# Kernel optimization log

Measured on AMD Instinct MI355X. Metric: run time of the kernel, lower is better.

The kernel has to match this reference:

```python
import jax, jax.numpy as jnp
import numpy as np

B, L, DIN, H, N, TEMB, NB = 16, 1024, 64, 256, 64, 128, 6


def setup_inputs() -> dict:
    key = jax.random.key(0)
    ks = jax.random.split(key, 16)
    def nrm(k, shape, scale):
        return jax.random.normal(k, shape, dtype=jnp.float32) * scale
    inp = {}
    inp["input"] = nrm(ks[0], (B, L, DIN), 1.0)
    inp["t"] = jax.random.uniform(ks[1], (B,), dtype=jnp.float32) * 1000.0
    inp["W_in"] = nrm(ks[2], (DIN, H), DIN ** -0.5)
    inp["b_in"] = jnp.zeros((H,), jnp.float32)
    inp["Wt1"] = nrm(ks[3], (TEMB, H), TEMB ** -0.5)
    inp["bt1"] = jnp.zeros((H,), jnp.float32)
    inp["Wt2"] = nrm(ks[4], (H, H), H ** -0.5)
    inp["bt2"] = jnp.zeros((H,), jnp.float32)
    inp["ln_g"] = jnp.ones((NB, H), jnp.float32)
    inp["ln_b"] = jnp.zeros((NB, H), jnp.float32)
    lo, hi = float(np.log(0.001)), float(np.log(0.1))
    inp["log_dt"] = jax.random.uniform(ks[5], (NB, H), dtype=jnp.float32) * (hi - lo) + lo
    inp["A_log_re"] = jnp.full((NB, H, N), float(np.log(0.5)), jnp.float32)
    inp["A_im"] = jnp.broadcast_to(np.pi * jnp.arange(N, dtype=jnp.float32), (NB, H, N)) + 0.0
    inp["C_re"] = nrm(ks[6], (NB, 2, H, N), 0.5 ** 0.5)
    inp["C_im"] = nrm(ks[7], (NB, 2, H, N), 0.5 ** 0.5)
    inp["Dp"] = nrm(ks[8], (NB, H), 1.0)
    inp["s4W"] = nrm(ks[9], (NB, H, H), H ** -0.5)
    inp["s4b"] = jnp.zeros((NB, H), jnp.float32)
    inp["tW"] = nrm(ks[10], (NB, H, H), H ** -0.5)
    inp["tb"] = jnp.zeros((NB, H), jnp.float32)
    inp["c1W"] = nrm(ks[11], (NB, H, H), H ** -0.5)
    inp["c1b"] = jnp.zeros((NB, H), jnp.float32)
    inp["c2W"] = nrm(ks[12], (NB, H, H), H ** -0.5)
    inp["c2b"] = jnp.zeros((NB, H), jnp.float32)
    inp["Wo1"] = nrm(ks[13], (H, H), H ** -0.5)
    inp["bo1"] = jnp.zeros((H,), jnp.float32)
    inp["Wo2"] = nrm(ks[14], (H, DIN), H ** -0.5)
    inp["bo2"] = jnp.zeros((DIN,), jnp.float32)
    return inp


def _sin_emb(t, dim):
    half = dim // 2
    freqs = jnp.exp(-np.log(10000.0) / (half - 1) * jnp.arange(half, dtype=jnp.float32))
    a = t[:, None] * freqs[None, :]
    return jnp.concatenate([jnp.sin(a), jnp.cos(a)], axis=-1)


def _forward(input, t, W_in, b_in, Wt1, bt1, Wt2, bt2, ln_g, ln_b, log_dt, A_log_re,
             A_im, C_re, C_im, Dp, s4W, s4b, tW, tb, c1W, c1b, c2W, c2b, Wo1, bo1, Wo2, bo2):
    x = jax.nn.relu(input @ W_in + b_in)                     # [B,L,H]
    tv = jax.nn.silu(_sin_emb(t, TEMB) @ Wt1 + bt1)
    tv = jax.nn.silu(tv @ Wt2 + bt2)                         # [B,H]
    x = jnp.swapaxes(x, -1, -2)                              # [B,H,L]
    length = x.shape[-1]
    nfft = 2 * length
    lgrid = jnp.arange(length)
    skips = jnp.zeros_like(x)
    for i in range(NB):
        # time conditioning (broadcast over L)
        tt = tv @ tW[i] + tb[i]                              # [B,H]
        z = x + tt[:, :, None]
        # LayerNorm over channel dim H
        zt = jnp.swapaxes(z, -1, -2)                         # [B,L,H]
        mu = zt.mean(-1, keepdims=True)
        var = zt.var(-1, keepdims=True)
        zn = (zt - mu) / jnp.sqrt(var + 1e-5) * ln_g[i] + ln_b[i]
        zn = jnp.swapaxes(zn, -1, -2)                        # [B,H,L]
        # S4 (diagonal ZOH) bidirectional convolution kernel
        dt = jnp.exp(log_dt[i])                              # [H]
        A = -jnp.exp(A_log_re[i]) + 1j * A_im[i]             # [H,N]
        dtA = A * dt[:, None]
        C = C_re[i] + 1j * C_im[i]                           # [2,H,N]
        dC = C * (jnp.exp(dtA) - 1.0) / A
        V = jnp.exp(dtA[:, :, None] * lgrid)                 # [H,N,L] Vandermonde
        K = 2.0 * jnp.einsum('shn,hnl->shl', dC, V).real     # [2,H,L]
        k = jnp.pad(K[0], ((0, 0), (0, length))) + jnp.pad(K[1][:, ::-1], ((0, 0), (length, 0)))
        y = jnp.fft.irfft(jnp.fft.rfft(zn, nfft) * jnp.fft.rfft(k, nfft)[None], nfft)[..., :length]
        y = y + zn * Dp[i][None, :, None]
        y = jax.nn.gelu(y, approximate=False)
        y = jnp.einsum('oh,bhl->bol', s4W[i], y) + s4b[i][None, :, None]
        out = y + z                                          # S4Layer residual
        g = jnp.tanh(out) * jax.nn.sigmoid(out)
        x = jnp.einsum('oh,bhl->bol', c1W[i], g) + c1b[i][None, :, None] + x
        skips = skips + jnp.einsum('oh,bhl->bol', c2W[i], g) + c2b[i][None, :, None]
    skip = jnp.swapaxes(skips, -1, -2)                       # [B,L,H]
    h = jax.nn.relu(skip @ Wo1 + bo1)
    out = h @ Wo2 + bo2
    return out + input                                       # init_skip


def reference(input, t, W_in, b_in, Wt1, bt1, Wt2, bt2, ln_g, ln_b, log_dt, A_log_re,
              A_im, C_re, C_im, Dp, s4W, s4b, tW, tb, c1W, c1b, c2W, c2b, Wo1, bo1, Wo2, bo2):
    return _forward(input, t, W_in, b_in, Wt1, bt1, Wt2, bt2, ln_g, ln_b, log_dt, A_log_re,
                    A_im, C_re, C_im, Dp, s4W, s4b, tW, tb, c1W, c1b, c2W, c2b, Wo1, bo1, Wo2, bo2)
```

## Files before the change

kernel.cpp:

```cpp
#include <hip/hip_runtime.h>
#include <math.h>


typedef __attribute__((ext_vector_type(8))) short bf16x8;
typedef __attribute__((ext_vector_type(4))) float f32x4;

__device__ __forceinline__ short f2bf(float f) {
  unsigned u = __builtin_bit_cast(unsigned, f);
  unsigned r = (u + 0x7FFFu + ((u >> 16) & 1u)) >> 16;
  return (short)r;
}
__device__ __forceinline__ float bf2f(unsigned short v) {
  unsigned u = ((unsigned)v) << 16;
  return __builtin_bit_cast(float, u);
}

__global__ __launch_bounds__(256) void k_temb(
    const float* __restrict__ t, const float* __restrict__ Wt1, const float* __restrict__ bt1,
    const float* __restrict__ Wt2, const float* __restrict__ bt2, float* __restrict__ tv) {
  int b = blockIdx.x, tid = threadIdx.x;
  __shared__ float emb[128];
  __shared__ float tv1[256];
  if (tid < 128) {
    int j = tid & 63;
    float f = expf(-logf(10000.f) / 63.f * (float)j);
    float a = t[b] * f;
    emb[tid] = (tid < 64) ? sinf(a) : cosf(a);
  }
  __syncthreads();
  float acc = bt1[tid];
  for (int k = 0; k < 128; k++) acc = fmaf(emb[k], Wt1[k * 256 + tid], acc);
  tv1[tid] = acc / (1.f + expf(-acc));
  __syncthreads();
  float acc2 = bt2[tid];
  for (int k = 0; k < 256; k++) acc2 = fmaf(tv1[k], Wt2[k * 256 + tid], acc2);
  tv[b * 256 + tid] = acc2 / (1.f + expf(-acc2));
}

__global__ __launch_bounds__(256) void k_tt(
    const float* __restrict__ tv, const float* __restrict__ tW, const float* __restrict__ tb,
    float* __restrict__ tt_all) {
  int i = blockIdx.x, b = blockIdx.y, h = threadIdx.x;
  __shared__ float s[256];
  s[h] = tv[b * 256 + h];
  __syncthreads();
  const float* W = tW + i * 256 * 256;
  float acc = tb[i * 256 + h];
  for (int k = 0; k < 256; k++) acc = fmaf(s[k], W[k * 256 + h], acc);
  tt_all[(i * 16 + b) * 256 + h] = acc;
}

__global__ __launch_bounds__(256) void k_in(
    const float* __restrict__ inp, const float* __restrict__ W, const float* __restrict__ bias,
    float* __restrict__ x) {
  int lt = blockIdx.x, b = blockIdx.y, h = threadIdx.x;
  __shared__ float si[64][68];
  int l0 = lt * 64;
  for (int rep = 0; rep < 16; rep++) {
    int idx = rep * 256 + h;
    int l = idx >> 6, d = idx & 63;
    si[l][d] = inp[(size_t)(b * 1024 + l0 + l) * 64 + d];
  }
  float wc[64];
  #pragma unroll
  for (int d = 0; d < 64; d++) wc[d] = W[d * 256 + h];
  float bh = bias[h];
  __syncthreads();
  float* xp = x + (size_t)(b * 256 + h) * 1024 + l0;
  for (int l4 = 0; l4 < 16; l4++) {
    float4 o;
    float* op = &o.x;
    #pragma unroll
    for (int j = 0; j < 4; j++) {
      int l = l4 * 4 + j;
      float a = bh;
      #pragma unroll
      for (int d4 = 0; d4 < 16; d4++) {
        float4 v = *reinterpret_cast<const float4*>(&si[l][d4 * 4]);
        a = fmaf(v.x, wc[d4 * 4 + 0], a);
        a = fmaf(v.y, wc[d4 * 4 + 1], a);
        a = fmaf(v.z, wc[d4 * 4 + 2], a);
        a = fmaf(v.w, wc[d4 * 4 + 3], a);
      }
      op[j] = fmaxf(a, 0.f);
    }
    *reinterpret_cast<float4*>(xp + l4 * 4) = o;
  }
}

__global__ __launch_bounds__(256) void k_tab(
    const float* __restrict__ log_dt, const float* __restrict__ A_log_re, const float* __restrict__ A_im,
    const float* __restrict__ C_re, const float* __restrict__ C_im,
    float* __restrict__ wtab, float* __restrict__ wTtab, float* __restrict__ dCtab) {
  int idx = blockIdx.x * 256 + threadIdx.x;
  int i = idx / (256 * 64);
  int rem = idx % (256 * 64);
  int h = rem >> 6, n = rem & 63;
  float dt = expf(log_dt[i * 256 + h]);
  float Ar = -expf(A_log_re[idx]);
  float Ai = A_im[idx];
  float ar = dt * Ar, ai = dt * Ai;
  float ea = expf(ar);
  float wr = ea * cosf(ai), wi = ea * sinf(ai);
  float pr = wr, pi = wi;
  #pragma unroll
  for (int s = 0; s < 6; s++) { float nr = pr * pr - pi * pi; float ni = 2.f * pr * pi; pr = nr; pi = ni; }
  float den = Ar * Ar + Ai * Ai;
  float qr = ((wr - 1.f) * Ar + wi * Ai) / den;
  float qi = (wi * Ar - (wr - 1.f) * Ai) / den;
  wtab[idx * 2] = wr; wtab[idx * 2 + 1] = wi;
  wTtab[idx * 2] = pr; wTtab[idx * 2 + 1] = pi;
  #pragma unroll
  for (int s = 0; s < 2; s++) {
    float cr = C_re[((size_t)(i * 2 + s) * 256 + h) * 64 + n];
    float ci = C_im[((size_t)(i * 2 + s) * 256 + h) * 64 + n];
    dCtab[(((size_t)(i * 2 + s) * 256 + h) * 64 + n) * 2]     = cr * qr - ci * qi;
    dCtab[(((size_t)(i * 2 + s) * 256 + h) * 64 + n) * 2 + 1] = cr * qi + ci * qr;
  }
}

__global__ __launch_bounds__(256) void k_prep(
    const float* __restrict__ s4W, const float* __restrict__ c1W, const float* __restrict__ c2W,
    const float* __restrict__ Wo1,
    unsigned short* __restrict__ s4Wbf, unsigned short* __restrict__ c12Wbf, unsigned short* __restrict__ Wo1T) {
  int idx = blockIdx.x * 256 + threadIdx.x;
  if (idx < 393216) {
    s4Wbf[idx] = (unsigned short)f2bf(s4W[idx]);
  } else if (idx < 393216 + 786432) {
    int j = idx - 393216;
    int i = j / 131072, r = j % 131072;
    int o2 = r >> 8, k = r & 255;
    float v = (o2 < 256) ? c1W[(size_t)i * 65536 + o2 * 256 + k]
                         : c2W[(size_t)i * 65536 + (o2 - 256) * 256 + k];
    c12Wbf[j] = (unsigned short)f2bf(v);
  } else {
    int j = idx - 1179648;
    int o = j >> 8, k = j & 255;
    Wo1T[j] = (unsigned short)f2bf(Wo1[k * 256 + o]);
  }
}

__global__ __launch_bounds__(256) void k_conv(const float* __restrict__ src, unsigned short* __restrict__ dst) {
  int idx = (blockIdx.x * 256 + threadIdx.x) * 8;
  float4 v0 = *reinterpret_cast<const float4*>(src + idx);
  float4 v1 = *reinterpret_cast<const float4*>(src + idx + 4);
  ushort4 a = make_ushort4((unsigned short)f2bf(v0.x), (unsigned short)f2bf(v0.y),
                           (unsigned short)f2bf(v0.z), (unsigned short)f2bf(v0.w));
  ushort4 b = make_ushort4((unsigned short)f2bf(v1.x), (unsigned short)f2bf(v1.y),
                           (unsigned short)f2bf(v1.z), (unsigned short)f2bf(v1.w));
  *reinterpret_cast<ushort4*>(dst + idx) = a;
  *reinterpret_cast<ushort4*>(dst + idx + 4) = b;
}

__global__ __launch_bounds__(256) void k_pcar(const float* __restrict__ wtab, float* __restrict__ Pt) {
  int idx = blockIdx.x * 256 + threadIdx.x;
  int i = idx >> 14, h = (idx >> 6) & 255, n = idx & 63;
  float wr = wtab[idx * 2], wi = wtab[idx * 2 + 1];
  float pr = 1.f, pi = 0.f;
  float* base = Pt + (size_t)i * 2097152 + (size_t)h * 8192 + 2 * n;
  for (int t = 0; t < 64; t++) {
    *reinterpret_cast<float2*>(base + t * 128) = make_float2(pr, -pi);
    float nr2 = pr * wr - pi * wi, ni2 = pr * wi + pi * wr;
    pr = nr2; pi = ni2;
  }
}

__global__ __launch_bounds__(256) void k_ktap(
    const float* __restrict__ dCtab, const float* __restrict__ Pt, float* __restrict__ Ktap) {
  int idx = blockIdx.x * 256 + threadIdx.x;
  int j = idx & 63;
  int h = (idx >> 6) & 255;
  int i = idx >> 15;
  const float* dc = dCtab + (size_t)(idx >> 6) * 128;
  const float* P = Pt + (size_t)i * 2097152 + (size_t)h * 8192 + j * 128;
  float acc = 0.f;
  for (int q = 0; q < 32; q++) {
    float4 d = *reinterpret_cast<const float4*>(dc + q * 4);
    float4 p = *reinterpret_cast<const float4*>(P + q * 4);
    acc = fmaf(d.x, p.x, fmaf(d.y, p.y, fmaf(d.z, p.z, fmaf(d.w, p.w, acc))));
  }
  Ktap[idx] = 2.f * acc;
}

__global__ __launch_bounds__(256) void k_ln(
    const float* __restrict__ x, const float* __restrict__ tt_all,
    const float* __restrict__ g, const float* __restrict__ bta, unsigned short* __restrict__ znbf, int i) {
  int ct = blockIdx.x, b = blockIdx.y, tid = threadIdx.x;
  __shared__ float tile[64][257];
  __shared__ float stt[256];
  __shared__ float red[8][64];
  __shared__ float mu_s[64], rs_s[64];
  stt[tid] = tt_all[(i * 16 + b) * 256 + tid];
  __syncthreads();
  int l0 = ct * 64;
  const float* xb = x + (size_t)(b * 256) * 1024 + l0;
  for (int rep = 0; rep < 16; rep++) {
    int idx = rep * 256 + tid;
    int h = idx >> 4;
    int l4 = (idx & 15) * 4;
    float4 v = *reinterpret_cast<const float4*>(xb + (size_t)h * 1024 + l4);
    float a = stt[h];
    tile[l4][h] = v.x + a; tile[l4 + 1][h] = v.y + a; tile[l4 + 2][h] = v.z + a; tile[l4 + 3][h] = v.w + a;
  }
  __syncthreads();
  int l = tid & 63, part = tid >> 6;
  float s1 = 0.f, s2 = 0.f;
  for (int k = 0; k < 64; k++) {
    float v = tile[l][part * 64 + k];
    s1 += v; s2 = fmaf(v, v, s2);
  }
  red[part][l] = s1; red[4 + part][l] = s2;
  __syncthreads();
  if (tid < 64) {
    float a = red[0][tid] + red[1][tid] + red[2][tid] + red[3][tid];
    float q = red[4][tid] + red[5][tid] + red[6][tid] + red[7][tid];
    float mu = a * (1.f / 256.f);
    float var = q * (1.f / 256.f) - mu * mu;
    mu_s[tid] = mu;
    rs_s[tid] = rsqrtf(var + 1e-5f);
  }
  __syncthreads();
  unsigned short* zb = znbf + (size_t)(b * 256) * 1024 + l0;
  for (int rep = 0; rep < 16; rep++) {
    int idx = rep * 256 + tid;
    int h = idx >> 4;
    int l4 = (idx & 15) * 4;
    float gg = g[i * 256 + h], bb2 = bta[i * 256 + h];
    float o0 = (tile[l4][h]     - mu_s[l4])     * rs_s[l4]     * gg + bb2;
    float o1 = (tile[l4 + 1][h] - mu_s[l4 + 1]) * rs_s[l4 + 1] * gg + bb2;
    float o2 = (tile[l4 + 2][h] - mu_s[l4 + 2]) * rs_s[l4 + 2] * gg + bb2;
    float o3 = (tile[l4 + 3][h] - mu_s[l4 + 3]) * rs_s[l4 + 3] * gg + bb2;
    ushort4 o4 = make_ushort4((unsigned short)f2bf(o0), (unsigned short)f2bf(o1),
                              (unsigned short)f2bf(o2), (unsigned short)f2bf(o3));
    *reinterpret_cast<ushort4*>(zb + (size_t)h * 1024 + l4) = o4;
  }
}

__global__ __launch_bounds__(512, 2) void k_bsc(
    const unsigned short* __restrict__ znbf, const float* __restrict__ Pt,
    const float* __restrict__ wtab, const float* __restrict__ wTtab, const float* __restrict__ dCtab,
    unsigned short* __restrict__ Bl, int i) {
  int h = blockIdx.x;
  int tid = threadIdx.x;
  __shared__ float Ps[64][130];
  __shared__ unsigned short Bp[256][72];
  {
    const float* src = Pt + (size_t)h * 8192;
    #pragma unroll
    for (int rep = 0; rep < 4; rep++) {
      int idx = rep * 512 + tid;
      int t = idx >> 5, k4 = (idx & 31) * 4;
      float4 v = *reinterpret_cast<const float4*>(src + t * 128 + k4);
      *reinterpret_cast<float4*>(&Ps[t][k4]) = v;
    }
  }
  __syncthreads();
  {
    int t = tid & 63;
    int colblk = tid >> 6;
    #pragma unroll
    for (int cc = 0; cc < 32; cc++) {
      int col = colblk * 32 + cc;
      int n = col & 63, comp = (col >> 6) & 1, dir = col >> 7;
      int k = 2 * n + comp;
      float v = dir ? Ps[t][k] : Ps[63 - t][k];
      if (comp) v = -v;
      Bp[col][t] = (unsigned short)f2bf(v);
    }
  }
  __syncthreads();

  int wid = tid >> 6, lane = tid & 63;
  int b = blockIdx.y * 8 + wid;
  int c = lane & 15, kq = lane >> 4;
  const unsigned short* pzn = znbf + ((size_t)(b * 256 + h)) * 1024 + c * 64 + kq * 8;

  bf16x8 af[2];
  af[0] = *reinterpret_cast<const bf16x8*>(pzn);
  af[1] = *reinterpret_cast<const bf16x8*>(pzn + 32);

  f32x4 acc[16];
  #pragma unroll
  for (int nt = 0; nt < 16; nt++) acc[nt] = (f32x4){0.f, 0.f, 0.f, 0.f};
  #pragma unroll
  for (int ks = 0; ks < 2; ks++) {
    #pragma unroll
    for (int nt = 0; nt < 16; nt++) {
      bf16x8 bfv = *reinterpret_cast<const bf16x8*>(&Bp[nt * 16 + c][ks * 32 + kq * 8]);
      acc[nt] = __builtin_amdgcn_mfma_f32_16x16x32_bf16(af[ks], bfv, acc[nt], 0, 0, 0);
    }
  }

  const int gib = (i * 256 + h) * 64;
  unsigned short* blf = Bl + ((size_t)(b * 256 + h)) * 2048;
  unsigned short* blb = blf + (size_t)4096 * 2048;

  #pragma unroll
  for (int j = 0; j < 4; j++) {
    int n = j * 16 + c;
    int gi = gib + n;
    float wTr = wTtab[gi * 2], wTi = wTtab[gi * 2 + 1];
    float w2r = wTr * wTr - wTi * wTi, w2i = 2.f * wTr * wTi;
    float w4r = w2r * w2r - w2i * w2i, w4i = 2.f * w2r * w2i;
    float w8r = w4r * w4r - w4i * w4i, w8i = 2.f * w4r * w4i;
    float wr = wtab[gi * 2], wi = wtab[gi * 2 + 1];
    float d0r = dCtab[((size_t)(i * 2 + 0) * 256 + h) * 128 + 2 * n];
    float d0i = dCtab[((size_t)(i * 2 + 0) * 256 + h) * 128 + 2 * n + 1];
    float d1r = dCtab[((size_t)(i * 2 + 1) * 256 + h) * 128 + 2 * n];
    float d1i = dCtab[((size_t)(i * 2 + 1) * 256 + h) * 128 + 2 * n + 1];
    float mfr = 2.f * (d0r * wr - d0i * wi), mfi = 2.f * (d0r * wi + d0i * wr);
    float mbr = 2.f * d1r, mbi = 2.f * d1i;

    {
      float er = 0.f, ei = 0.f, entr[4], enti[4];
      #pragma unroll
      for (int r = 0; r < 4; r++) {
        entr[r] = er; enti[r] = ei;
        float br = acc[j][r], bi = acc[j + 4][r];
        float t0 = er * wTr - ei * wTi + br;
        ei = er * wTi + ei * wTr + bi; er = t0;
      }
      float Gr = er, Gi = ei;
      float sr = __shfl_up(Gr, 16), si = __shfl_up(Gi, 16);
      if (kq >= 1) { Gr += sr * w4r - si * w4i; Gi += sr * w4i + si * w4r; }
      sr = __shfl_up(Gr, 32); si = __shfl_up(Gi, 32);
      if (kq >= 2) { Gr += sr * w8r - si * w8i; Gi += sr * w8i + si * w8r; }
      float Sgr = __shfl_up(Gr, 16), Sgi = __shfl_up(Gi, 16);
      if (kq == 0) { Sgr = 0.f; Sgi = 0.f; }
      float pr = 1.f, pi = 0.f;
      #pragma unroll
      for (int r = 0; r < 4; r++) {
        float scr = pr * Sgr - pi * Sgi + entr[r];
        float sci = pr * Sgi + pi * Sgr + enti[r];
        float opr = mfr * scr - mfi * sci;
        float opi = mfr * sci + mfi * scr;
        *reinterpret_cast<ushort2*>(blf + (size_t)(kq * 4 + r) * 128 + 2 * n) =
            make_ushort2((unsigned short)f2bf(opr), (unsigned short)f2bf(opi));
        float t0 = pr * wTr - pi * wTi; pi = pr * wTi + pi * wTr; pr = t0;
      }
    }
    {
      float er = 0.f, ei = 0.f, entr[4], enti[4];
      #pragma unroll
      for (int rr = 0; rr < 4; rr++) {
        int r = 3 - rr;
        entr[r] = er; enti[r] = ei;
        float br = acc[8 + j][r], bi = acc[12 + j][r];
        float t0 = er * wTr - ei * wTi + br;
        ei = er * wTi + ei * wTr + bi; er = t0;
      }
      float Gr = er, Gi = ei;
      float sr = __shfl_down(Gr, 16), si = __shfl_down(Gi, 16);
      if (kq <= 2) { Gr += sr * w4r - si * w4i; Gi += sr * w4i + si * w4r; }
      sr = __shfl_down(Gr, 32); si = __shfl_down(Gi, 32);
      if (kq <= 1) { Gr += sr * w8r - si * w8i; Gi += sr * w8i + si * w8r; }
      float Sgr = __shfl_down(Gr, 16), Sgi = __shfl_down(Gi, 16);
      if (kq == 3) { Sgr = 0.f; Sgi = 0.f; }
      float pr = 1.f, pi = 0.f;
      #pragma unroll
      for (int rr = 0; rr < 4; rr++) {
        int r = 3 - rr;
        float scr = pr * Sgr - pi * Sgi + entr[r];
        float sci = pr * Sgi + pi * Sgr + enti[r];
        float opr = mbr * scr - mbi * sci;
        float opi = mbr * sci + mbi * scr;
        *reinterpret_cast<ushort2*>(blb + (size_t)(kq * 4 + r) * 128 + 2 * n) =
            make_ushort2((unsigned short)f2bf(opr), (unsigned short)f2bf(opi));
        float t0 = pr * wTr - pi * wTi; pi = pr * wTi + pi * wTr; pr = t0;
      }
    }
  }
}

__global__ __launch_bounds__(512) void k_apply(
    const unsigned short* __restrict__ znbf, const unsigned short* __restrict__ Bl,
    const float* __restrict__ Pt, const float* __restrict__ Ktap, const float* __restrict__ Dp,
    unsigned short* __restrict__ ygbf, int i) {
  int h = blockIdx.x;
  int tid = threadIdx.x;
  __shared__ short Blds[64][344];
  __shared__ float k0s[64], k1s[64];
  if (tid < 64) k0s[tid] = Ktap[(0 * 256 + h) * 64 + tid];
  else if (tid < 128) k1s[tid - 64] = Ktap[(1 * 256 + h) * 64 + (tid - 64)];
  __syncthreads();
  {
    int trow = tid >> 6, klane = tid & 63;
    const float* Pth = Pt + (size_t)h * 8192;
    #pragma unroll
    for (int ti = 0; ti < 8; ti++) {
      int t = ti * 8 + trow;
      #pragma unroll
      for (int kc = 0; kc < 5; kc++) {
        int k = kc * 64 + klane;
        float v;
        if (kc < 2)      v = Pth[t * 128 + k];
        else if (kc < 4) v = Pth[(63 - t) * 128 + (k - 128)];
        else {
          int tp = klane;
          v = (t >= tp) ? k0s[t - tp] : k1s[tp - t - 1];
        }
        Blds[t][k] = f2bf(v);
      }
    }
  }
  __syncthreads();

  int wid = tid >> 6, lane = tid & 63;
  int b = blockIdx.y * 8 + wid;
  int c = lane & 15, kq = lane >> 4;
  const unsigned short* pa0 = Bl + ((size_t)(b * 256 + h)) * 2048 + c * 128 + kq * 8;
  const unsigned short* pa1 = pa0 + (size_t)4096 * 2048;
  const unsigned short* pzn = znbf + ((size_t)(b * 256 + h)) * 1024 + c * 64 + kq * 8;

  f32x4 acc[4];
  #pragma unroll
  for (int nt = 0; nt < 4; nt++) acc[nt] = (f32x4){0.f, 0.f, 0.f, 0.f};

  #pragma unroll
  for (int ks = 0; ks < 10; ks++) {
    bf16x8 af;
    if (ks < 4)       af = *reinterpret_cast<const bf16x8*>(pa0 + ks * 32);
    else if (ks < 8)  af = *reinterpret_cast<const bf16x8*>(pa1 + (ks - 4) * 32);
    else              af = *reinterpret_cast<const bf16x8*>(pzn + (ks - 8) * 32);
    #pragma unroll
    for (int nt = 0; nt < 4; nt++) {
      bf16x8 bfv = *reinterpret_cast<const bf16x8*>(&Blds[nt * 16 + c][ks * 32 + kq * 8]);
      acc[nt] = __builtin_amdgcn_mfma_f32_16x16x32_bf16(af, bfv, acc[nt], 0, 0, 0);
    }
  }

  float dp = Dp[i * 256 + h];
  size_t obase = (size_t)(b * 256 + h) * 1024;
  #pragma unroll
  for (int nt = 0; nt < 4; nt++) {
    #pragma unroll
    for (int r = 0; r < 4; r++) {
      int m = kq * 4 + r;
      int t = nt * 16 + c;
      size_t idx = obase + (size_t)m * 64 + t;
      float z = bf2f(znbf[idx]);
      float v = fmaf(z, dp, acc[nt][r]);
      float gel = 0.5f * v * (1.f + erff(v * 0.70710678118f));
      ygbf[idx] = (unsigned short)f2bf(gel);
    }
  }
}

template <int EPI>
__global__ __launch_bounds__(256) void k_gemm(
    const unsigned short* __restrict__ Wbf, const float* __restrict__ bias1, const float* __restrict__ bias2,
    const unsigned short* __restrict__ act, float* __restrict__ out1, float* __restrict__ out2,
    unsigned short* __restrict__ outb, const float* __restrict__ aux1, const float* __restrict__ aux2) {
  int lt = blockIdx.x, ot = blockIdx.y, b = blockIdx.z;
  int tid = threadIdx.x;
  int l0 = lt * 128, o0 = ot * 64;
  __shared__ unsigned short Alds[128 * 40];

  int wid = tid >> 6, lane = tid & 63;
  int wo = wid >> 1, wl = wid & 1;
  int c = lane & 15, kq = lane >> 4;

  int kq4 = tid >> 5;
  int lq = tid & 31;
  const unsigned short* actb = act + (size_t)(b * 256) * 1024 + l0 + lq * 4;

  f32x4 acc[2][4];
  #pragma unroll
  for (int mo = 0; mo < 2; mo++)
    #pragma unroll
    for (int nl = 0; nl < 4; nl++) acc[mo][nl] = (f32x4){0.f, 0.f, 0.f, 0.f};

  ushort4 m0, m1, m2, m3;
  {
    const unsigned short* p = actb + (size_t)(kq4 * 4) * 1024;
    m0 = *reinterpret_cast<const ushort4*>(p);
    m1 = *reinterpret_cast<const ushort4*>(p + 1024);
    m2 = *reinterpret_cast<const ushort4*>(p + 2048);
    m3 = *reinterpret_cast<const ushort4*>(p + 3072);
  }

  for (int kc = 0; kc < 256; kc += 32) {
    {
      int g0 = kq4 >> 1, hh = (kq4 & 1) * 4;
      int rot = (g0 + lq) & 3;
      unsigned short* wp = &Alds[(lq * 4) * 40 + rot * 8 + hh];
      ushort4 w;
      w = make_ushort4(m0.x, m1.x, m2.x, m3.x); *reinterpret_cast<ushort4*>(wp) = w;
      w = make_ushort4(m0.y, m1.y, m2.y, m3.y); *reinterpret_cast<ushort4*>(wp + 40) = w;
      w = make_ushort4(m0.z, m1.z, m2.z, m3.z); *reinterpret_cast<ushort4*>(wp + 80) = w;
      w = make_ushort4(m0.w, m1.w, m2.w, m3.w); *reinterpret_cast<ushort4*>(wp + 120) = w;
    }
    __syncthreads();
    {
      int kcn = (kc + 32) & 255;
      const unsigned short* p = actb + (size_t)(kcn + kq4 * 4) * 1024;
      m0 = *reinterpret_cast<const ushort4*>(p);
      m1 = *reinterpret_cast<const ushort4*>(p + 1024);
      m2 = *reinterpret_cast<const ushort4*>(p + 2048);
      m3 = *reinterpret_cast<const ushort4*>(p + 3072);
    }
    bf16x8 af[2];
    #pragma unroll
    for (int mo = 0; mo < 2; mo++) {
      const unsigned short* wp = Wbf + (size_t)(o0 + wo * 32 + mo * 16 + c) * 256 + kc + kq * 8;
      af[mo] = *reinterpret_cast<const bf16x8*>(wp);
    }
    bf16x8 bfr[4];
    #pragma unroll
    for (int nl = 0; nl < 4; nl++) {
      int l = wl * 64 + nl * 16 + c;
      int rot = (kq + (l >> 2)) & 3;
      bfr[nl] = *reinterpret_cast<const bf16x8*>(&Alds[l * 40 + rot * 8]);
    }
    #pragma unroll
    for (int mo = 0; mo < 2; mo++)
      #pragma unroll
      for (int nl = 0; nl < 4; nl++)
        acc[mo][nl] = __builtin_amdgcn_mfma_f32_16x16x32_bf16(af[mo], bfr[nl], acc[mo][nl], 0, 0, 0);
    __syncthreads();
  }

  #pragma unroll
  for (int mo = 0; mo < 2; mo++) {
    #pragma unroll
    for (int nl = 0; nl < 4; nl++) {
      #pragma unroll
      for (int r = 0; r < 4; r++) {
        float a = acc[mo][nl][r];
        int o = o0 + wo * 32 + mo * 16 + kq * 4 + r;
        int l = l0 + wl * 64 + nl * 16 + c;
        if constexpr (EPI == 0) {
          size_t id = ((size_t)(b * 256 + o)) * 1024 + l;
          float u = a + bias1[o] + aux1[id] + aux2[b * 256 + o];
          float t = __expf(fminf(-u, 80.f));
          float gg = (1.f - t) / (1.f + t * t);
          outb[id] = (unsigned short)f2bf(gg);
        } else if constexpr (EPI == 1 || EPI == 4) {
          if (o < 256) {
            size_t id = ((size_t)(b * 256 + o)) * 1024 + l;
            out1[id] += a + bias1[o];
          } else {
            int o2 = o - 256;
            size_t id = ((size_t)(b * 256 + o2)) * 1024 + l;
            if constexpr (EPI == 4) out2[id] = a + bias2[o2];
            else                    out2[id] += a + bias2[o2];
          }
        } else {
          size_t id = ((size_t)(b * 256 + o)) * 1024 + l;
          out1[id] = fmaxf(a + bias1[o], 0.f);
        }
      }
    }
  }
}

__global__ __launch_bounds__(256) void k_out(
    const float* __restrict__ h1, const float* __restrict__ Wo2, const float* __restrict__ bo2,
    const float* __restrict__ inp, float* __restrict__ outp) {
  int lt = blockIdx.x, b = blockIdx.y, tid = threadIdx.x;
  __shared__ float sa[32][132];
  __shared__ float sw2[32][68];
  int l0 = lt * 128;
  float acc[4][8];
  #pragma unroll
  for (int r = 0; r < 4; r++)
    #pragma unroll
    for (int c2 = 0; c2 < 8; c2++) acc[r][c2] = 0.f;
  int df = (tid & 7) * 8;
  int lf = (tid >> 3) * 4;
  for (int kc = 0; kc < 256; kc += 32) {
    for (int rep = 0; rep < 4; rep++) {
      int idx = rep * 256 + tid;
      int kk = idx >> 5;
      int l4 = (idx & 31) * 4;
      float4 v = *reinterpret_cast<const float4*>(h1 + (size_t)(b * 256 + kc + kk) * 1024 + l0 + l4);
      *reinterpret_cast<float4*>(&sa[kk][l4]) = v;
    }
    for (int rep = 0; rep < 8; rep++) {
      int idx = rep * 256 + tid;
      int kk = idx >> 6, d = idx & 63;
      sw2[kk][d] = Wo2[(size_t)(kc + kk) * 64 + d];
    }
    __syncthreads();
    for (int kk = 0; kk < 32; kk++) {
      float4 av = *reinterpret_cast<const float4*>(&sa[kk][lf]);
      float4 w1 = *reinterpret_cast<const float4*>(&sw2[kk][df]);
      float4 w2 = *reinterpret_cast<const float4*>(&sw2[kk][df + 4]);
      float avv[4] = {av.x, av.y, av.z, av.w};
      float wv[8] = {w1.x, w1.y, w1.z, w1.w, w2.x, w2.y, w2.z, w2.w};
      #pragma unroll
      for (int r = 0; r < 4; r++)
        #pragma unroll
        for (int c2 = 0; c2 < 8; c2++) acc[r][c2] = fmaf(avv[r], wv[c2], acc[r][c2]);
    }
    __syncthreads();
  }
  float bv[8];
  #pragma unroll
  for (int c2 = 0; c2 < 8; c2++) bv[c2] = bo2[df + c2];
  #pragma unroll
  for (int r = 0; r < 4; r++) {
    size_t base = (size_t)(b * 1024 + l0 + lf + r) * 64 + df;
    float4 i1 = *reinterpret_cast<const float4*>(inp + base);
    float4 i2 = *reinterpret_cast<const float4*>(inp + base + 4);
    float4 o1 = make_float4(acc[r][0] + bv[0] + i1.x, acc[r][1] + bv[1] + i1.y,
                            acc[r][2] + bv[2] + i1.z, acc[r][3] + bv[3] + i1.w);
    float4 o2 = make_float4(acc[r][4] + bv[4] + i2.x, acc[r][5] + bv[5] + i2.y,
                            acc[r][6] + bv[6] + i2.z, acc[r][7] + bv[7] + i2.w);
    *reinterpret_cast<float4*>(outp + base) = o1;
    *reinterpret_cast<float4*>(outp + base + 4) = o2;
  }
}

extern "C" void kernel_launch(void* const* d_in, const int* in_sizes, int n_in,
                              void* d_out, int out_size, void* d_ws, size_t ws_size,
                              hipStream_t stream) {
  const float* input   = (const float*)d_in[0];
  const float* t       = (const float*)d_in[1];
  const float* W_in    = (const float*)d_in[2];
  const float* b_in    = (const float*)d_in[3];
  const float* Wt1     = (const float*)d_in[4];
  const float* bt1     = (const float*)d_in[5];
  const float* Wt2     = (const float*)d_in[6];
  const float* bt2     = (const float*)d_in[7];
  const float* ln_g    = (const float*)d_in[8];
  const float* ln_b    = (const float*)d_in[9];
  const float* log_dt  = (const float*)d_in[10];
  const float* A_log_re= (const float*)d_in[11];
  const float* A_im    = (const float*)d_in[12];
  const float* C_re    = (const float*)d_in[13];
  const float* C_im    = (const float*)d_in[14];
  const float* Dp      = (const float*)d_in[15];
  const float* s4W     = (const float*)d_in[16];
  const float* s4b     = (const float*)d_in[17];
  const float* tW      = (const float*)d_in[18];
  const float* tb      = (const float*)d_in[19];
  const float* c1W     = (const float*)d_in[20];
  const float* c1b     = (const float*)d_in[21];
  const float* c2W     = (const float*)d_in[22];
  const float* c2b     = (const float*)d_in[23];
  const float* Wo1     = (const float*)d_in[24];
  const float* bo1     = (const float*)d_in[25];
  const float* Wo2     = (const float*)d_in[26];
  const float* bo2     = (const float*)d_in[27];

  float* ws = (float*)d_ws;
  size_t off = 0;
  float* x      = ws + off; off += 4194304;
  float* zn     = ws + off; off += 4194304;
  float* ygbuf  = ws + off; off += 4194304;
  float* skips  = ws + off; off += 4194304;
  float* tv     = ws + off; off += 4096;
  float* tt_all = ws + off; off += 24576;
  float* wtab   = ws + off; off += 196608;
  float* wTtab  = ws + off; off += 196608;
  float* dCtab  = ws + off; off += 393216;
  float* Pt     = ws + off; off += 12582912;
  float* Ktap   = ws + off; off += 196608;
  float* Bl     = ws + off; off += 8388608;
  unsigned short* s4Wbf  = (unsigned short*)(ws + off); off += 196608;
  unsigned short* c12Wbf = (unsigned short*)(ws + off); off += 393216;
  unsigned short* Wo1T   = (unsigned short*)(ws + off); off += 32768;

  unsigned short* Blb     = (unsigned short*)Bl;
  unsigned short* znbf    = (unsigned short*)zn;
  unsigned short* ygbf    = (unsigned short*)ygbuf;
  unsigned short* gbf     = (unsigned short*)(ygbuf + 2097152);
  unsigned short* skipsbf = (unsigned short*)x;
  float* h1 = zn;

  k_temb<<<16, 256, 0, stream>>>(t, Wt1, bt1, Wt2, bt2, tv);
  k_tt<<<dim3(6, 16), 256, 0, stream>>>(tv, tW, tb, tt_all);
  k_in<<<dim3(16, 16), 256, 0, stream>>>(input, W_in, b_in, x);
  k_tab<<<384, 256, 0, stream>>>(log_dt, A_log_re, A_im, C_re, C_im, wtab, wTtab, dCtab);
  k_prep<<<4864, 256, 0, stream>>>(s4W, c1W, c2W, Wo1, s4Wbf, c12Wbf, Wo1T);
  k_pcar<<<384, 256, 0, stream>>>(wtab, Pt);
  k_ktap<<<768, 256, 0, stream>>>(dCtab, Pt, Ktap);

  for (int i = 0; i < 6; i++) {
    k_ln<<<dim3(16, 16), 256, 0, stream>>>(x, tt_all, ln_g, ln_b, znbf, i);
    k_bsc<<<dim3(256, 2), 512, 0, stream>>>(znbf, Pt + (size_t)i * 2097152, wtab, wTtab, dCtab, Blb, i);
    k_apply<<<dim3(256, 2), 512, 0, stream>>>(znbf, Blb, Pt + (size_t)i * 2097152,
                                              Ktap + (size_t)i * 32768, Dp, ygbf, i);
    k_gemm<0><<<dim3(8, 4, 16), 256, 0, stream>>>(s4Wbf + (size_t)i * 65536, s4b + i * 256, nullptr,
                                                  ygbf, nullptr, nullptr, gbf, x, tt_all + i * 4096);
    if (i == 0)
      k_gemm<4><<<dim3(8, 8, 16), 256, 0, stream>>>(c12Wbf, c1b, c2b, gbf, x, skips,
                                                    nullptr, nullptr, nullptr);
    else
      k_gemm<1><<<dim3(8, 8, 16), 256, 0, stream>>>(c12Wbf + (size_t)i * 131072, c1b + i * 256,
                                                    c2b + i * 256, gbf, x, skips,
                                                    nullptr, nullptr, nullptr);
  }
  k_conv<<<2048, 256, 0, stream>>>(skips, skipsbf);
  k_gemm<2><<<dim3(8, 4, 16), 256, 0, stream>>>(Wo1T, bo1, nullptr,
                                                skipsbf, h1, nullptr, nullptr, nullptr, nullptr);
  k_out<<<dim3(8, 16), 256, 0, stream>>>(h1, Wo2, bo2, input, (float*)d_out);
}
```

Baseline: 597.8 us.

## Fuse chunked-scan state kernel into apply kernel, keeping states in LDS

Merges the k_bsc boundary-state kernel and the k_apply output kernel into one k_s4 kernel per layer. The per-chunk scan states now stay in shared memory (Sw) instead of round-tripping through a large global Bl buffer, and the propagator table Pt is read from global once and held in LDS as bf16 for both phases, with the XR buffer reused between phases. This removes one launch per layer and the global write and read of the intermediate states. In exchange the block uses much more shared memory and is limited to one block per CU (launch bounds 512,1), so occupancy drops.

```diff
diff --git a/kernel.cpp b/kernel.cpp
--- a/kernel.cpp
+++ b/kernel.cpp
@@ -236,14 +236,21 @@
   }
 }
 
-__global__ __launch_bounds__(512, 2) void k_bsc(
+__global__ __launch_bounds__(512, 1) void k_s4(
     const unsigned short* __restrict__ znbf, const float* __restrict__ Pt,
     const float* __restrict__ wtab, const float* __restrict__ wTtab, const float* __restrict__ dCtab,
-    unsigned short* __restrict__ Bl, int i) {
+    const float* __restrict__ Ktap, const float* __restrict__ Dp,
+    unsigned short* __restrict__ ygbf, int i) {
   int h = blockIdx.x;
   int tid = threadIdx.x;
-  __shared__ float Ps[64][130];
-  __shared__ unsigned short Bp[256][72];
+  __shared__ unsigned short Psb[64][130];
+  __shared__ unsigned short XR[22016];
+  __shared__ unsigned short Sw[8][2][16][136];
+  __shared__ float k0s[64], k1s[64];
+
+  if (tid < 64) k0s[tid] = Ktap[h * 64 + tid];
+  else if (tid < 128) k1s[tid - 64] = Ktap[16384 + h * 64 + (tid - 64)];
+
   {
     const float* src = Pt + (size_t)h * 8192;
     #pragma unroll
@@ -251,7 +258,10 @@
       int idx = rep * 512 + tid;
       int t = idx >> 5, k4 = (idx & 31) * 4;
       float4 v = *reinterpret_cast<const float4*>(src + t * 128 + k4);
-      *reinterpret_cast<float4*>(&Ps[t][k4]) = v;
+      ushort2 a = make_ushort2((unsigned short)f2bf(v.x), (unsigned short)f2bf(v.y));
+      ushort2 bq = make_ushort2((unsigned short)f2bf(v.z), (unsigned short)f2bf(v.w));
+      *reinterpret_cast<ushort2*>(&Psb[t][k4]) = a;
+      *reinterpret_cast<ushort2*>(&Psb[t][k4 + 2]) = bq;
     }
   }
   __syncthreads();
@@ -263,9 +273,9 @@
       int col = colblk * 32 + cc;
       int n = col & 63, comp = (col >> 6) & 1, dir = col >> 7;
       int k = 2 * n + comp;
-      float v = dir ? Ps[t][k] : Ps[63 - t][k];
-      if (comp) v = -v;
-      Bp[col][t] = (unsigned short)f2bf(v);
+      unsigned short v = dir ? Psb[t][k] : Psb[63 - t][k];
+      if (comp) v ^= 0x8000u;
+      XR[col * 72 + t] = v;
     }
   }
   __syncthreads();
@@ -275,26 +285,48 @@
   int c = lane & 15, kq = lane >> 4;
   const unsigned short* pzn = znbf + ((size_t)(b * 256 + h)) * 1024 + c * 64 + kq * 8;
 
-  bf16x8 af[2];
-  af[0] = *reinterpret_cast<const bf16x8*>(pzn);
-  af[1] = *reinterpret_cast<const bf16x8*>(pzn + 32);
+  bf16x8 af0 = *reinterpret_cast<const bf16x8*>(pzn);
+  bf16x8 af1 = *reinterpret_cast<const bf16x8*>(pzn + 32);
 
   f32x4 acc[16];
   #pragma unroll
   for (int nt = 0; nt < 16; nt++) acc[nt] = (f32x4){0.f, 0.f, 0.f, 0.f};
   #pragma unroll
-  for (int ks = 0; ks < 2; ks++) {
-    #pragma unroll
-    for (int nt = 0; nt < 16; nt++) {
-      bf16x8 bfv = *reinterpret_cast<const bf16x8*>(&Bp[nt * 16 + c][ks * 32 + kq * 8]);
-      acc[nt] = __builtin_amdgcn_mfma_f32_16x16x32_bf16(af[ks], bfv, acc[nt], 0, 0, 0);
-    }
-  }
-
+  for (int nt = 0; nt < 16; nt++) {
+    bf16x8 b0 = *reinterpret_cast<const bf16x8*>(&XR[(nt * 16 + c) * 72 + kq * 8]);
+    acc[nt] = __builtin_amdgcn_mfma_f32_16x16x32_bf16(af0, b0, acc[nt], 0, 0, 0);
+  }
+  #pragma unroll
+  for (int nt = 0; nt < 16; nt++) {
+    bf16x8 b1 = *reinterpret_cast<const bf16x8*>(&XR[(nt * 16 + c) * 72 + 32 + kq * 8]);
+    acc[nt] = __builtin_amdgcn_mfma_f32_16x16x32_bf16(af1, b1, acc[nt], 0, 0, 0);
+  }
+  __syncthreads();
+
+  {
+    int trow = tid >> 6, klane = tid & 63;
+    #pragma unroll
+    for (int ti = 0; ti < 8; ti++) {
+      int t = ti * 8 + trow;
+      #pragma unroll
+      for (int kc = 0; kc < 5; kc++) {
+        int k = kc * 64 + klane;
+        unsigned short v;
+        if (kc < 2)      v = Psb[t][k];
+        else if (kc < 4) v = Psb[63 - t][k - 128];
+        else {
+          int tp = klane;
+          float f = (t >= tp) ? k0s[t - tp] : k1s[tp - t - 1];
+          v = (unsigned short)f2bf(f);
+        }
+        XR[t * 344 + k] = v;
+      }
+    }
+  }
+
+  unsigned short* swf = &Sw[wid][0][0][0];
+  unsigned short* swb = &Sw[wid][1][0][0];
   const int gib = (i * 256 + h) * 64;
-  unsigned short* blf = Bl + ((size_t)(b * 256 + h)) * 2048;
-  unsigned short* blb = blf + (size_t)4096 * 2048;
-
   #pragma unroll
   for (int j = 0; j < 4; j++) {
     int n = j * 16 + c;
@@ -334,7 +366,7 @@
         float sci = pr * Sgi + pi * Sgr + enti[r];
         float opr = mfr * scr - mfi * sci;
         float opi = mfr * sci + mfi * scr;
-        *reinterpret_cast<ushort2*>(blf + (size_t)(kq * 4 + r) * 128 + 2 * n) =
+        *reinterpret_cast<ushort2*>(swf + (kq * 4 + r) * 136 + 2 * n) =
             make_ushort2((unsigned short)f2bf(opr), (unsigned short)f2bf(opi));
         float t0 = pr * wTr - pi * wTi; pi = pr * wTi + pi * wTr; pr = t0;
       }
@@ -364,68 +396,27 @@
         float sci = pr * Sgi + pi * Sgr + enti[r];
         float opr = mbr * scr - mbi * sci;
         float opi = mbr * sci + mbi * scr;
-        *reinterpret_cast<ushort2*>(blb + (size_t)(kq * 4 + r) * 128 + 2 * n) =
+        *reinterpret_cast<ushort2*>(swb + (kq * 4 + r) * 136 + 2 * n) =
             make_ushort2((unsigned short)f2bf(opr), (unsigned short)f2bf(opi));
         float t0 = pr * wTr - pi * wTi; pi = pr * wTi + pi * wTr; pr = t0;
       }
     }
   }
-}
-
-__global__ __launch_bounds__(512) void k_apply(
-    const unsigned short* __restrict__ znbf, const unsigned short* __restrict__ Bl,
-    const float* __restrict__ Pt, const float* __restrict__ Ktap, const float* __restrict__ Dp,
-    unsigned short* __restrict__ ygbf, int i) {
-  int h = blockIdx.x;
-  int tid = threadIdx.x;
-  __shared__ short Blds[64][344];
-  __shared__ float k0s[64], k1s[64];
-  if (tid < 64) k0s[tid] = Ktap[(0 * 256 + h) * 64 + tid];
-  else if (tid < 128) k1s[tid - 64] = Ktap[(1 * 256 + h) * 64 + (tid - 64)];
-  __syncthreads();
-  {
-    int trow = tid >> 6, klane = tid & 63;
-    const float* Pth = Pt + (size_t)h * 8192;
-    #pragma unroll
-    for (int ti = 0; ti < 8; ti++) {
-      int t = ti * 8 + trow;
-      #pragma unroll
-      for (int kc = 0; kc < 5; kc++) {
-        int k = kc * 64 + klane;
-        float v;
-        if (kc < 2)      v = Pth[t * 128 + k];
-        else if (kc < 4) v = Pth[(63 - t) * 128 + (k - 128)];
-        else {
-          int tp = klane;
-          v = (t >= tp) ? k0s[t - tp] : k1s[tp - t - 1];
-        }
-        Blds[t][k] = f2bf(v);
-      }
-    }
-  }
-  __syncthreads();
-
-  int wid = tid >> 6, lane = tid & 63;
-  int b = blockIdx.y * 8 + wid;
-  int c = lane & 15, kq = lane >> 4;
-  const unsigned short* pa0 = Bl + ((size_t)(b * 256 + h)) * 2048 + c * 128 + kq * 8;
-  const unsigned short* pa1 = pa0 + (size_t)4096 * 2048;
-  const unsigned short* pzn = znbf + ((size_t)(b * 256 + h)) * 1024 + c * 64 + kq * 8;
-
-  f32x4 acc[4];
-  #pragma unroll
-  for (int nt = 0; nt < 4; nt++) acc[nt] = (f32x4){0.f, 0.f, 0.f, 0.f};
-
+  __syncthreads();
+
+  f32x4 acc2[4];
+  #pragma unroll
+  for (int nt = 0; nt < 4; nt++) acc2[nt] = (f32x4){0.f, 0.f, 0.f, 0.f};
   #pragma unroll
   for (int ks = 0; ks < 10; ks++) {
     bf16x8 af;
-    if (ks < 4)       af = *reinterpret_cast<const bf16x8*>(pa0 + ks * 32);
-    else if (ks < 8)  af = *reinterpret_cast<const bf16x8*>(pa1 + (ks - 4) * 32);
+    if (ks < 4)       af = *reinterpret_cast<const bf16x8*>(swf + c * 136 + ks * 32 + kq * 8);
+    else if (ks < 8)  af = *reinterpret_cast<const bf16x8*>(swb + c * 136 + (ks - 4) * 32 + kq * 8);
     else              af = *reinterpret_cast<const bf16x8*>(pzn + (ks - 8) * 32);
     #pragma unroll
     for (int nt = 0; nt < 4; nt++) {
-      bf16x8 bfv = *reinterpret_cast<const bf16x8*>(&Blds[nt * 16 + c][ks * 32 + kq * 8]);
-      acc[nt] = __builtin_amdgcn_mfma_f32_16x16x32_bf16(af, bfv, acc[nt], 0, 0, 0);
+      bf16x8 bfv = *reinterpret_cast<const bf16x8*>(&XR[(nt * 16 + c) * 344 + ks * 32 + kq * 8]);
+      acc2[nt] = __builtin_amdgcn_mfma_f32_16x16x32_bf16(af, bfv, acc2[nt], 0, 0, 0);
     }
   }
 
@@ -439,7 +430,7 @@
       int t = nt * 16 + c;
       size_t idx = obase + (size_t)m * 64 + t;
       float z = bf2f(znbf[idx]);
-      float v = fmaf(z, dp, acc[nt][r]);
+      float v = fmaf(z, dp, acc2[nt][r]);
       float gel = 0.5f * v * (1.f + erff(v * 0.70710678118f));
       ygbf[idx] = (unsigned short)f2bf(gel);
     }
@@ -657,12 +648,10 @@
   float* dCtab  = ws + off; off += 393216;
   float* Pt     = ws + off; off += 12582912;
   float* Ktap   = ws + off; off += 196608;
-  float* Bl     = ws + off; off += 8388608;
   unsigned short* s4Wbf  = (unsigned short*)(ws + off); off += 196608;
   unsigned short* c12Wbf = (unsigned short*)(ws + off); off += 393216;
   unsigned short* Wo1T   = (unsigned short*)(ws + off); off += 32768;
 
-  unsigned short* Blb     = (unsigned short*)Bl;
   unsigned short* znbf    = (unsigned short*)zn;
   unsigned short* ygbf    = (unsigned short*)ygbuf;
   unsigned short* gbf     = (unsigned short*)(ygbuf + 2097152);
@@ -679,9 +668,8 @@
 
   for (int i = 0; i < 6; i++) {
     k_ln<<<dim3(16, 16), 256, 0, stream>>>(x, tt_all, ln_g, ln_b, znbf, i);
-    k_bsc<<<dim3(256, 2), 512, 0, stream>>>(znbf, Pt + (size_t)i * 2097152, wtab, wTtab, dCtab, Blb, i);
-    k_apply<<<dim3(256, 2), 512, 0, stream>>>(znbf, Blb, Pt + (size_t)i * 2097152,
-                                              Ktap + (size_t)i * 32768, Dp, ygbf, i);
+    k_s4<<<dim3(256, 2), 512, 0, stream>>>(znbf, Pt + (size_t)i * 2097152, wtab, wTtab, dCtab,
+                                           Ktap + (size_t)i * 32768, Dp, ygbf, i);
     k_gemm<0><<<dim3(8, 4, 16), 256, 0, stream>>>(s4Wbf + (size_t)i * 65536, s4b + i * 256, nullptr,
                                                   ygbf, nullptr, nullptr, gbf, x, tt_all + i * 4096);
     if (i == 0)
```

Result: faster. 580.2 us (-3.0%).
